# Optimization experiments

Hardware: AMD Instinct MI355X
Metric: run time of the kernel (lower is better)

## Reference

```python
import jax, jax.numpy as jnp
import numpy as np

B = 2048          # batch_size
D = 512           # embedding dim
TEMP = 0.1        # temperature
EPS = 1e-8        # torch CosineSimilarity eps


def _neg_idx(batch_size):
    n = 2 * batch_size
    mask = np.eye(n) + np.eye(n, n, k=-batch_size) + np.eye(n, n, k=batch_size)
    mask = (1 - mask).astype(bool)           # True at negatives
    # each row has exactly n-2 True entries -> fixed-shape gather indices
    return np.nonzero(mask)[1].reshape(n, n - 2)

_NEG_IDX = jnp.asarray(_neg_idx(B))           # [2B, 2B-2]
_ROWS = jnp.arange(2 * B)[:, None]            # [2B, 1]


def _cos_sim_matrix(r):
    # r: [2B, D] -> [2B, 2B] cosine similarity
    norm = jnp.maximum(jnp.linalg.norm(r, axis=-1, keepdims=True), EPS)
    rn = r / norm
    return rn @ rn.T


def _pos(sim):
    # diag(sim, +B) and diag(sim, -B), concatenated -> [2B, 1]
    l = jnp.diagonal(sim, offset=B)
    r = jnp.diagonal(sim, offset=-B)
    return jnp.concatenate([l, r])[:, None]


def _neg(sim):
    # masked gather of off-(diag,+B,-B) entries -> [2B, 2B-2]
    return sim[_ROWS, _NEG_IDX]


def _ce_sum_label0(logits):
    # CrossEntropyLoss(reduction='sum') with all labels == 0
    return -jnp.sum(jax.nn.log_softmax(logits, axis=-1)[:, 0])


def setup_inputs() -> dict:
    key = jax.random.key(0)
    k1, k2, k3, k4 = jax.random.split(key, 4)
    return {
        "z_ori": jax.random.normal(k1, (B, D), jnp.float32),
        "z_hard_pos": jax.random.normal(k2, (B, D), jnp.float32),
        "z_soft_pos": jax.random.normal(k3, (B, D), jnp.float32),
        "z_soft_neg": jax.random.normal(k4, (B, D), jnp.float32),
    }


def reference(z_ori, z_hard_pos, z_soft_pos, z_soft_neg):
    sim_ori_hp = _cos_sim_matrix(jnp.concatenate([z_ori, z_hard_pos], axis=0))
    sim_ori_sp = _cos_sim_matrix(jnp.concatenate([z_ori, z_soft_pos], axis=0))
    sim_ori_sn = _cos_sim_matrix(jnp.concatenate([z_ori, z_soft_neg], axis=0))
    sim_hp_sp = _cos_sim_matrix(jnp.concatenate([z_hard_pos, z_soft_pos], axis=0))
    sim_hp_sn = _cos_sim_matrix(jnp.concatenate([z_hard_pos, z_soft_neg], axis=0))
    sim_sp_sn = _cos_sim_matrix(jnp.concatenate([z_soft_pos, z_soft_neg], axis=0))

    pos_ori_sn = _pos(sim_ori_sn)
    pos_hp_sn = _pos(sim_hp_sn)
    pos_sp_sn = _pos(sim_sp_sn)

    pos_ori_hp = _pos(sim_ori_hp)
    neg_ori_hp = _neg(sim_ori_hp)
    pos_ori_sp = _pos(sim_ori_sp)
    neg_ori_sp = _neg(sim_ori_sp)
    pos_hp_sp = _pos(sim_hp_sp)
    neg_hp_sp = _neg(sim_hp_sp)

    logits_ori_hp = jnp.concatenate([pos_ori_hp, neg_ori_hp, pos_ori_sn], axis=1) / TEMP
    logits_ori_sp = jnp.concatenate([pos_ori_sp, neg_ori_sp, pos_ori_sn], axis=1) / TEMP
    logits_hp_sp = jnp.concatenate([pos_hp_sp, neg_hp_sp, pos_hp_sn, pos_sp_sn], axis=1) / TEMP

    denom = 2.0 * B
    return (
        _ce_sum_label0(logits_ori_hp) / denom,
        _ce_sum_label0(logits_ori_sp) / denom,
        _ce_sum_label0(logits_hp_sp) / denom,
    )
```

## Files before the change

### kernel.cpp

```cpp
#include <hip/hip_runtime.h>
#include <hip/hip_bf16.h>

#define Bn 2048
#define Dn 512

typedef float f32x4 __attribute__((ext_vector_type(4)));

typedef __attribute__((address_space(1))) const unsigned int gas_u32;
typedef __attribute__((address_space(3))) unsigned int las_u32;

__device__ __forceinline__ void gload16(const void* g, void* l) {
  __builtin_amdgcn_global_load_lds((gas_u32*)g, (las_u32*)l, 16, 0, 0);
}

__global__ __launch_bounds__(256) void normalize_kernel(
    const float* __restrict__ in0, const float* __restrict__ in1,
    const float* __restrict__ in2, const float* __restrict__ in3,
    unsigned char* __restrict__ nm8, float* __restrict__ rs, float* __restrict__ dd) {
  __shared__ float sv[4][Dn];
  __shared__ float red[4][6];
  int row = blockIdx.x;
  int wave = threadIdx.x >> 6, lane = threadIdx.x & 63;

  int g = blockIdx.x * 256 + threadIdx.x;
  if (g < 9 * Bn) rs[g] = 0.0f;

  const float* src =
      (wave == 0 ? in0 : wave == 1 ? in1 : wave == 2 ? in2 : in3) + (size_t)row * Dn;
  int k = lane * 8;
  float4 x0 = *(const float4*)(src + k);
  float4 x1 = *(const float4*)(src + k + 4);
  float v[8] = {x0.x, x0.y, x0.z, x0.w, x1.x, x1.y, x1.z, x1.w};
  float ss = 0.f;
#pragma unroll
  for (int e = 0; e < 8; e++) ss = fmaf(v[e], v[e], ss);
#pragma unroll
  for (int off = 1; off < 64; off <<= 1) ss += __shfl_xor(ss, off, 64);
  float scale = 1.0f / fmaxf(sqrtf(ss), 1e-8f);
  float nv[8];
#pragma unroll
  for (int e = 0; e < 8; e++) {
    nv[e] = v[e] * scale;
    sv[wave][k + e] = nv[e];
  }
  if (wave < 3) {
    unsigned int lo = __builtin_amdgcn_cvt_pk_fp8_f32(nv[0], nv[1], 0u, false);
    lo = __builtin_amdgcn_cvt_pk_fp8_f32(nv[2], nv[3], lo, true);
    unsigned int hi = __builtin_amdgcn_cvt_pk_fp8_f32(nv[4], nv[5], 0u, false);
    hi = __builtin_amdgcn_cvt_pk_fp8_f32(nv[6], nv[7], hi, true);
    uint2 pk; pk.x = lo; pk.y = hi;
    *(uint2*)(nm8 + ((size_t)wave * Bn + row) * Dn + k) = pk;
  }
  __syncthreads();

  int t = threadIdx.x;
  float o0 = sv[0][2 * t], o1 = sv[0][2 * t + 1];
  float h0 = sv[1][2 * t], h1 = sv[1][2 * t + 1];
  float p0 = sv[2][2 * t], p1 = sv[2][2 * t + 1];
  float n0 = sv[3][2 * t], n1 = sv[3][2 * t + 1];
  float s[6];
  s[0] = fmaf(o0, h0, o1 * h1);
  s[1] = fmaf(o0, p0, o1 * p1);
  s[2] = fmaf(h0, p0, h1 * p1);
  s[3] = fmaf(o0, n0, o1 * n1);
  s[4] = fmaf(h0, n0, h1 * n1);
  s[5] = fmaf(p0, n0, p1 * n1);
#pragma unroll
  for (int off = 1; off < 64; off <<= 1) {
#pragma unroll
    for (int j = 0; j < 6; j++) s[j] += __shfl_xor(s[j], off, 64);
  }
  if (lane == 0) {
#pragma unroll
    for (int j = 0; j < 6; j++) red[wave][j] = s[j];
  }
  __syncthreads();
  if (threadIdx.x < 6) {
    int j = threadIdx.x;
    dd[j * Bn + row] = red[0][j] + red[1][j] + red[2][j] + red[3][j];
  }
}

#define GBM 128
#define GBK 64
#define NKT 8
#define NBUF 3

__global__ __launch_bounds__(512, 6) void gemm_fp8_kernel(const unsigned char* __restrict__ nm8,
                                                          float* __restrict__ rs) {
  __shared__ unsigned char lds[NBUF * 16384];

  int id = ((int)blockIdx.x & 7) * 147 + ((int)blockIdx.x >> 3);
  int by = 0, rem = id, cnt = 48;
  while (rem >= cnt) { rem -= cnt; by++; cnt--; }
  int bx = by + rem;
  int u = by >> 4, v = bx >> 4;
  int rrow, rcol;
  if (u == v) { rrow = u; rcol = u; }
  else if (u == 0) { if (v == 1) { rrow = 3; rcol = 4; } else { rrow = 5; rcol = 6; } }
  else { rrow = 7; rcol = 8; }

  const unsigned char* gA = nm8 + ((size_t)u * Bn + (size_t)(by & 15) * GBM) * Dn;
  const unsigned char* gB = nm8 + ((size_t)v * Bn + (size_t)(bx & 15) * GBM) * Dn;

  int tid = threadIdx.x, lane = tid & 63, wave = tid >> 6;
  int wr = wave >> 2, wc = wave & 3;
  int c = lane & 15, rgrp = lane >> 4;
  int xc = ((c >> 1) & 3) << 1;

  int srow = tid >> 2;
  int sx = ((srow >> 1) & 3) << 1;
  int su = ((tid & 3) << 1) ^ sx;
  const unsigned char* sA = gA + (size_t)srow * Dn + su * 8;
  const unsigned char* sB = gB + (size_t)srow * Dn + su * 8;
  int woff = wave << 10;

  f32x4 acc[4][2] = {};

  gload16(sA, lds + woff);
  gload16(sB, lds + 8192 + woff);
  gload16(sA + GBK, lds + 16384 + woff);
  gload16(sB + GBK, lds + 16384 + 8192 + woff);
  asm volatile("s_waitcnt vmcnt(2)" ::: "memory");
  __builtin_amdgcn_s_barrier();
  asm volatile("" ::: "memory");

#pragma unroll
  for (int t = 0; t < NKT; ++t) {
    const int j = t % NBUF;
    const unsigned char* As = lds + j * 16384;
    const unsigned char* Bs = As + 8192;
    long long a[2][4], b[2][2];
#pragma unroll
    for (int ks = 0; ks < 2; ++ks) {
      int ub = (ks * 4 + rgrp) ^ xc;
#pragma unroll
      for (int mi = 0; mi < 4; ++mi)
        a[ks][mi] = *(const long long*)(As + (wr * 64 + mi * 16 + c) * 64 + ub * 8);
#pragma unroll
      for (int ni = 0; ni < 2; ++ni)
        b[ks][ni] = *(const long long*)(Bs + (wc * 32 + ni * 16 + c) * 64 + ub * 8);
    }
    if (t + 2 < NKT) {
      const int j2 = (t + 2) % NBUF;
      gload16(sA + (t + 2) * GBK, lds + j2 * 16384 + woff);
      gload16(sB + (t + 2) * GBK, lds + j2 * 16384 + 8192 + woff);
    }
    __builtin_amdgcn_s_setprio(1);
#pragma unroll
    for (int ks = 0; ks < 2; ++ks)
#pragma unroll
      for (int mi = 0; mi < 4; ++mi)
#pragma unroll
        for (int ni = 0; ni < 2; ++ni)
          acc[mi][ni] =
              __builtin_amdgcn_mfma_f32_16x16x32_fp8_fp8(a[ks][mi], b[ks][ni], acc[mi][ni], 0, 0, 0);
    __builtin_amdgcn_s_setprio(0);
    if (t + 2 < NKT) {
      asm volatile("s_waitcnt vmcnt(2)" ::: "memory");
    } else if (t == NKT - 2) {
      asm volatile("s_waitcnt vmcnt(0)" ::: "memory");
    }
    __builtin_amdgcn_s_barrier();
    asm volatile("" ::: "memory");
    __builtin_amdgcn_sched_barrier(0);
  }

  float* crow = (float*)lds;
  float* ccol = crow + GBM;
  __syncthreads();
  if (tid < 2 * GBM) ((float*)lds)[tid] = 0.0f;
  __syncthreads();

  bool skip_diag = (by == bx);
#pragma unroll
  for (int mi = 0; mi < 4; ++mi)
#pragma unroll
    for (int ni = 0; ni < 2; ++ni)
#pragma unroll
      for (int r = 0; r < 4; ++r) {
        int lrow = wr * 64 + mi * 16 + rgrp * 4 + r;
        int lcol = wc * 32 + ni * 16 + c;
        float e = __expf(10.0f * acc[mi][ni][r] - 10.0f);
        acc[mi][ni][r] = (skip_diag && lrow == lcol) ? 0.0f : e;
      }

#pragma unroll
  for (int mi = 0; mi < 4; ++mi)
#pragma unroll
    for (int r = 0; r < 4; ++r) {
      float val = acc[mi][0][r] + acc[mi][1][r];
      val += __shfl_xor(val, 1, 64);
      val += __shfl_xor(val, 2, 64);
      val += __shfl_xor(val, 4, 64);
      val += __shfl_xor(val, 8, 64);
      if (c == 0) atomicAdd(&crow[wr * 64 + mi * 16 + rgrp * 4 + r], val);
    }
#pragma unroll
  for (int ni = 0; ni < 2; ++ni) {
    float cv = 0.f;
#pragma unroll
    for (int mi = 0; mi < 4; ++mi)
#pragma unroll
      for (int r = 0; r < 4; ++r) cv += acc[mi][ni][r];
    cv += __shfl_xor(cv, 16, 64);
    cv += __shfl_xor(cv, 32, 64);
    if (lane < 16) atomicAdd(&ccol[wc * 32 + ni * 16 + c], cv);
  }
  __syncthreads();

  float* rs_row = rs + rrow * Bn + (by & 15) * GBM;
  if (tid < GBM) {
    atomicAdd(rs_row + tid, crow[tid]);
  } else if (tid < 2 * GBM && by != bx) {
    float* rs_col = rs + rcol * Bn + (bx & 15) * GBM;
    atomicAdd(rs_col + (tid - GBM), ccol[tid - GBM]);
  }
}

__global__ __launch_bounds__(1024) void final_kernel(const float* __restrict__ rs,
                                                     const float* __restrict__ dd,
                                                     float* __restrict__ out) {
  int tid = threadIdx.x;
  float l1 = 0.f, l2 = 0.f, l3 = 0.f;
  for (int i = tid; i < Bn; i += 1024) {
    float doh = dd[i], dop = dd[Bn + i], dhp = dd[2 * Bn + i];
    float ea = __expf(10.0f * dd[3 * Bn + i] - 10.0f);
    float eb = __expf(10.0f * dd[4 * Bn + i] - 10.0f);
    float ec = __expf(10.0f * dd[5 * Bn + i] - 10.0f);
    float r0 = rs[i], r1 = rs[Bn + i], r2 = rs[2 * Bn + i];
    float r3 = rs[3 * Bn + i], r4 = rs[4 * Bn + i], r5 = rs[5 * Bn + i];
    float r6 = rs[6 * Bn + i], r7 = rs[7 * Bn + i], r8 = rs[8 * Bn + i];
    l1 += 20.0f + logf(r0 + r3 + ea) + logf(r4 + r1 + ea) - 20.0f * doh;
    l2 += 20.0f + logf(r0 + r5 + ea) + logf(r6 + r2 + ea) - 20.0f * dop;
    l3 += 20.0f + logf(r1 + r7 + eb + ec) + logf(r8 + r2 + eb + ec) - 20.0f * dhp;
  }
  __shared__ float red[3][1024];
  red[0][tid] = l1; red[1][tid] = l2; red[2][tid] = l3;
  __syncthreads();
  for (int s = 512; s > 0; s >>= 1) {
    if (tid < s) {
      red[0][tid] += red[0][tid + s];
      red[1][tid] += red[1][tid + s];
      red[2][tid] += red[2][tid + s];
    }
    __syncthreads();
  }
  if (tid == 0) {
    out[0] = red[0][0] / 4096.0f;
    out[1] = red[1][0] / 4096.0f;
    out[2] = red[2][0] / 4096.0f;
  }
}

extern "C" void kernel_launch(void* const* d_in, const int* in_sizes, int n_in,
                              void* d_out, int out_size, void* d_ws, size_t ws_size,
                              hipStream_t stream) {
  const float* z0 = (const float*)d_in[0];
  const float* z1 = (const float*)d_in[1];
  const float* z2 = (const float*)d_in[2];
  const float* z3 = (const float*)d_in[3];
  float* out = (float*)d_out;

  unsigned char* nm8 = (unsigned char*)d_ws;
  float* rs = (float*)((char*)d_ws + (size_t)3 * Bn * Dn);
  float* dd = rs + 9 * Bn;

  hipLaunchKernelGGL(normalize_kernel, dim3(2048), dim3(256), 0, stream,
                     z0, z1, z2, z3, nm8, rs, dd);
  hipLaunchKernelGGL(gemm_fp8_kernel, dim3(1176), dim3(512), 0, stream, nm8, rs);
  hipLaunchKernelGGL(final_kernel, dim3(1), dim3(1024), 0, stream, rs, dd, out);
}
```

Before: 47.78 us.

## Enlarge FP8 GEMM tile to 256x256 with interleaved per-k-step MFMA scheduling

Doubles the GEMM block tile from 128x128 to 256x256, so each block holds an 8x4 accumulator grid per wave and loads four 16-byte chunks per stage. This cuts the grid from 1176 to 300 blocks and halves global/LDS traffic per output. The LDS fragment loads and MFMAs are now interleaved per k-substep, and blocks are remapped across XCDs. The cost is much higher register and LDS use (occupancy hint lowered to 2) and coarser load balance: 300 blocks on roughly 256 CUs leaves a partial second wave.

```diff
diff --git a/kernel.cpp b/kernel.cpp
--- a/kernel.cpp
+++ b/kernel.cpp
@@ -81,27 +81,30 @@
   }
 }
 
-#define GBM 128
+#define GBM 256
 #define GBK 64
 #define NKT 8
 #define NBUF 3
 
-__global__ __launch_bounds__(512, 6) void gemm_fp8_kernel(const unsigned char* __restrict__ nm8,
+__global__ __launch_bounds__(512, 2) void gemm_fp8_kernel(const unsigned char* __restrict__ nm8,
                                                           float* __restrict__ rs) {
-  __shared__ unsigned char lds[NBUF * 16384];
-
-  int id = ((int)blockIdx.x & 7) * 147 + ((int)blockIdx.x >> 3);
-  int by = 0, rem = id, cnt = 48;
+  __shared__ unsigned char lds[NBUF * 32768];
+
+  int orig = (int)blockIdx.x;
+  int xcd = orig & 7;
+  int id = (xcd < 4 ? xcd * 38 : 152 + (xcd - 4) * 37) + (orig >> 3);
+
+  int by = 0, rem = id, cnt = 24;
   while (rem >= cnt) { rem -= cnt; by++; cnt--; }
   int bx = by + rem;
-  int u = by >> 4, v = bx >> 4;
+  int u = by >> 3, v = bx >> 3;
   int rrow, rcol;
   if (u == v) { rrow = u; rcol = u; }
   else if (u == 0) { if (v == 1) { rrow = 3; rcol = 4; } else { rrow = 5; rcol = 6; } }
   else { rrow = 7; rcol = 8; }
 
-  const unsigned char* gA = nm8 + ((size_t)u * Bn + (size_t)(by & 15) * GBM) * Dn;
-  const unsigned char* gB = nm8 + ((size_t)v * Bn + (size_t)(bx & 15) * GBM) * Dn;
+  const unsigned char* gA = nm8 + ((size_t)u * Bn + (size_t)(by & 7) * GBM) * Dn;
+  const unsigned char* gB = nm8 + ((size_t)v * Bn + (size_t)(bx & 7) * GBM) * Dn;
 
   int tid = threadIdx.x, lane = tid & 63, wave = tid >> 6;
   int wr = wave >> 2, wc = wave & 3;
@@ -109,111 +112,113 @@
   int xc = ((c >> 1) & 3) << 1;
 
   int srow = tid >> 2;
-  int sx = ((srow >> 1) & 3) << 1;
-  int su = ((tid & 3) << 1) ^ sx;
-  const unsigned char* sA = gA + (size_t)srow * Dn + su * 8;
-  const unsigned char* sB = gB + (size_t)srow * Dn + su * 8;
-  int woff = wave << 10;
-
-  f32x4 acc[4][2] = {};
-
-  gload16(sA, lds + woff);
-  gload16(sB, lds + 8192 + woff);
-  gload16(sA + GBK, lds + 16384 + woff);
-  gload16(sB + GBK, lds + 16384 + 8192 + woff);
-  asm volatile("s_waitcnt vmcnt(2)" ::: "memory");
+  int suu = (tid & 3) ^ ((srow >> 1) & 3);
+  size_t aoff = (size_t)srow * Dn + suu * 16;
+  const unsigned char* sA = gA + aoff;
+  const unsigned char* sB = gB + aoff;
+  int dbase = wave << 10;
+
+#define STAGE(kt, j)                                                              \
+  {                                                                               \
+    unsigned char* d = lds + (j) * 32768;                                         \
+    gload16(sA + (kt) * GBK, d + dbase);                                          \
+    gload16(sA + (kt) * GBK + (size_t)128 * Dn, d + 8192 + dbase);                \
+    gload16(sB + (kt) * GBK, d + 16384 + dbase);                                  \
+    gload16(sB + (kt) * GBK + (size_t)128 * Dn, d + 16384 + 8192 + dbase);        \
+  }
+
+  f32x4 acc[8][4] = {};
+
+  STAGE(0, 0);
+  STAGE(1, 1);
+  asm volatile("s_waitcnt vmcnt(4)" ::: "memory");
   __builtin_amdgcn_s_barrier();
   asm volatile("" ::: "memory");
 
 #pragma unroll
   for (int t = 0; t < NKT; ++t) {
     const int j = t % NBUF;
-    const unsigned char* As = lds + j * 16384;
-    const unsigned char* Bs = As + 8192;
-    long long a[2][4], b[2][2];
+    const unsigned char* As = lds + j * 32768;
+    const unsigned char* Bs = As + 16384;
+    if (t + 2 < NKT) STAGE(t + 2, (t + 2) % NBUF);
 #pragma unroll
     for (int ks = 0; ks < 2; ++ks) {
-      int ub = (ks * 4 + rgrp) ^ xc;
-#pragma unroll
-      for (int mi = 0; mi < 4; ++mi)
-        a[ks][mi] = *(const long long*)(As + (wr * 64 + mi * 16 + c) * 64 + ub * 8);
-#pragma unroll
-      for (int ni = 0; ni < 2; ++ni)
-        b[ks][ni] = *(const long long*)(Bs + (wc * 32 + ni * 16 + c) * 64 + ub * 8);
+      int ub = ((ks * 4 + rgrp) ^ xc) << 3;
+      long long a[8], b[4];
+#pragma unroll
+      for (int mi = 0; mi < 8; ++mi)
+        a[mi] = *(const long long*)(As + (wr * 128 + mi * 16 + c) * 64 + ub);
+#pragma unroll
+      for (int ni = 0; ni < 4; ++ni)
+        b[ni] = *(const long long*)(Bs + (wc * 64 + ni * 16 + c) * 64 + ub);
+      __builtin_amdgcn_s_setprio(1);
+#pragma unroll
+      for (int mi = 0; mi < 8; ++mi)
+#pragma unroll
+        for (int ni = 0; ni < 4; ++ni)
+          acc[mi][ni] =
+              __builtin_amdgcn_mfma_f32_16x16x32_fp8_fp8(a[mi], b[ni], acc[mi][ni], 0, 0, 0);
+      __builtin_amdgcn_s_setprio(0);
     }
     if (t + 2 < NKT) {
-      const int j2 = (t + 2) % NBUF;
-      gload16(sA + (t + 2) * GBK, lds + j2 * 16384 + woff);
-      gload16(sB + (t + 2) * GBK, lds + j2 * 16384 + 8192 + woff);
-    }
-    __builtin_amdgcn_s_setprio(1);
-#pragma unroll
-    for (int ks = 0; ks < 2; ++ks)
-#pragma unroll
-      for (int mi = 0; mi < 4; ++mi)
-#pragma unroll
-        for (int ni = 0; ni < 2; ++ni)
-          acc[mi][ni] =
-              __builtin_amdgcn_mfma_f32_16x16x32_fp8_fp8(a[ks][mi], b[ks][ni], acc[mi][ni], 0, 0, 0);
-    __builtin_amdgcn_s_setprio(0);
-    if (t + 2 < NKT) {
-      asm volatile("s_waitcnt vmcnt(2)" ::: "memory");
-    } else if (t == NKT - 2) {
+      asm volatile("s_waitcnt vmcnt(4)" ::: "memory");
+    } else if (t + 1 < NKT) {
       asm volatile("s_waitcnt vmcnt(0)" ::: "memory");
     }
     __builtin_amdgcn_s_barrier();
     asm volatile("" ::: "memory");
     __builtin_amdgcn_sched_barrier(0);
   }
+#undef STAGE
 
   float* crow = (float*)lds;
   float* ccol = crow + GBM;
   __syncthreads();
-  if (tid < 2 * GBM) ((float*)lds)[tid] = 0.0f;
+  ((float*)lds)[tid] = 0.0f;
   __syncthreads();
 
   bool skip_diag = (by == bx);
 #pragma unroll
-  for (int mi = 0; mi < 4; ++mi)
-#pragma unroll
-    for (int ni = 0; ni < 2; ++ni)
+  for (int mi = 0; mi < 8; ++mi)
+#pragma unroll
+    for (int ni = 0; ni < 4; ++ni)
 #pragma unroll
       for (int r = 0; r < 4; ++r) {
-        int lrow = wr * 64 + mi * 16 + rgrp * 4 + r;
-        int lcol = wc * 32 + ni * 16 + c;
+        int lrow = wr * 128 + mi * 16 + rgrp * 4 + r;
+        int lcol = wc * 64 + ni * 16 + c;
         float e = __expf(10.0f * acc[mi][ni][r] - 10.0f);
         acc[mi][ni][r] = (skip_diag && lrow == lcol) ? 0.0f : e;
       }
 
 #pragma unroll
-  for (int mi = 0; mi < 4; ++mi)
+  for (int mi = 0; mi < 8; ++mi)
 #pragma unroll
     for (int r = 0; r < 4; ++r) {
-      float val = acc[mi][0][r] + acc[mi][1][r];
+      float val = acc[mi][0][r] + acc[mi][1][r] + acc[mi][2][r] + acc[mi][3][r];
       val += __shfl_xor(val, 1, 64);
       val += __shfl_xor(val, 2, 64);
       val += __shfl_xor(val, 4, 64);
       val += __shfl_xor(val, 8, 64);
-      if (c == 0) atomicAdd(&crow[wr * 64 + mi * 16 + rgrp * 4 + r], val);
-    }
-#pragma unroll
-  for (int ni = 0; ni < 2; ++ni) {
+      if (c == 0) atomicAdd(&crow[wr * 128 + mi * 16 + rgrp * 4 + r], val);
+    }
+#pragma unroll
+  for (int ni = 0; ni < 4; ++ni) {
     float cv = 0.f;
 #pragma unroll
-    for (int mi = 0; mi < 4; ++mi)
+    for (int mi = 0; mi < 8; ++mi)
 #pragma unroll
       for (int r = 0; r < 4; ++r) cv += acc[mi][ni][r];
     cv += __shfl_xor(cv, 16, 64);
     cv += __shfl_xor(cv, 32, 64);
-    if (lane < 16) atomicAdd(&ccol[wc * 32 + ni * 16 + c], cv);
-  }
-  __syncthreads();
-
-  float* rs_row = rs + rrow * Bn + (by & 15) * GBM;
+    if (lane < 16) atomicAdd(&ccol[wc * 64 + ni * 16 + c], cv);
+  }
+  __syncthreads();
+
+  float* rs_row = rs + rrow * Bn + (by & 7) * GBM;
   if (tid < GBM) {
     atomicAdd(rs_row + tid, crow[tid]);
-  } else if (tid < 2 * GBM && by != bx) {
-    float* rs_col = rs + rcol * Bn + (bx & 15) * GBM;
+  } else if (by != bx) {
+    float* rs_col = rs + rcol * Bn + (bx & 7) * GBM;
     atomicAdd(rs_col + (tid - GBM), ccol[tid - GBM]);
   }
 }
@@ -268,6 +273,6 @@
 
   hipLaunchKernelGGL(normalize_kernel, dim3(2048), dim3(256), 0, stream,
                      z0, z1, z2, z3, nm8, rs, dd);
-  hipLaunchKernelGGL(gemm_fp8_kernel, dim3(1176), dim3(512), 0, stream, nm8, rs);
+  hipLaunchKernelGGL(gemm_fp8_kernel, dim3(300), dim3(512), 0, stream, nm8, rs);
   hipLaunchKernelGGL(final_kernel, dim3(1), dim3(1024), 0, stream, rs, dd, out);
 }
```

Result: slower. 55.45 us (+16.0%).

## Permute fp8 layout for 16-byte LDS reads and deepen prefetch to four buffers

Applied to the files above, without the earlier changes.

The normalize kernel now writes fp8 rows in a permuted order within each 64-byte k-block, so each lane's two k-substeps sit next to each other. The GEMM can then fetch its A and B fragments with one 16-byte LDS read instead of two 8-byte reads, using a matching XOR swizzle. The pipeline grows from three to four LDS buffers with prefetch distance three, and the occupancy hint in launch_bounds is dropped. The goal is fewer LDS instructions and better hiding of global-to-LDS latency, at the cost of more LDS per block and possibly fewer resident blocks.

```diff
diff --git a/kernel.cpp b/kernel.cpp
--- a/kernel.cpp
+++ b/kernel.cpp
@@ -5,6 +5,7 @@
 #define Dn 512
 
 typedef float f32x4 __attribute__((ext_vector_type(4)));
+typedef long long ll2 __attribute__((ext_vector_type(2)));
 
 typedef __attribute__((address_space(1))) const unsigned int gas_u32;
 typedef __attribute__((address_space(3))) unsigned int las_u32;
@@ -22,8 +23,8 @@
   int row = blockIdx.x;
   int wave = threadIdx.x >> 6, lane = threadIdx.x & 63;
 
-  int g = blockIdx.x * 256 + threadIdx.x;
-  if (g < 9 * Bn) rs[g] = 0.0f;
+  int g0 = blockIdx.x * 256 + threadIdx.x;
+  if (g0 < 9 * Bn) rs[g0] = 0.0f;
 
   const float* src =
       (wave == 0 ? in0 : wave == 1 ? in1 : wave == 2 ? in2 : in3) + (size_t)row * Dn;
@@ -49,7 +50,9 @@
     unsigned int hi = __builtin_amdgcn_cvt_pk_fp8_f32(nv[4], nv[5], 0u, false);
     hi = __builtin_amdgcn_cvt_pk_fp8_f32(nv[6], nv[7], hi, true);
     uint2 pk; pk.x = lo; pk.y = hi;
-    *(uint2*)(nm8 + ((size_t)wave * Bn + row) * Dn + k) = pk;
+    int kb = lane >> 3, g = lane & 7;
+    int p = ((g & 3) << 1) | (g >> 2);
+    *(uint2*)(nm8 + ((size_t)wave * Bn + row) * Dn + kb * 64 + p * 8) = pk;
   }
   __syncthreads();
 
@@ -84,10 +87,10 @@
 #define GBM 128
 #define GBK 64
 #define NKT 8
-#define NBUF 3
-
-__global__ __launch_bounds__(512, 6) void gemm_fp8_kernel(const unsigned char* __restrict__ nm8,
-                                                          float* __restrict__ rs) {
+#define NBUF 4
+
+__global__ __launch_bounds__(512) void gemm_fp8_kernel(const unsigned char* __restrict__ nm8,
+                                                       float* __restrict__ rs) {
   __shared__ unsigned char lds[NBUF * 16384];
 
   int id = ((int)blockIdx.x & 7) * 147 + ((int)blockIdx.x >> 3);
@@ -106,46 +109,44 @@
   int tid = threadIdx.x, lane = tid & 63, wave = tid >> 6;
   int wr = wave >> 2, wc = wave & 3;
   int c = lane & 15, rgrp = lane >> 4;
-  int xc = ((c >> 1) & 3) << 1;
+  int ru = ((rgrp ^ ((c >> 1) & 3)) << 4);
 
   int srow = tid >> 2;
-  int sx = ((srow >> 1) & 3) << 1;
-  int su = ((tid & 3) << 1) ^ sx;
-  const unsigned char* sA = gA + (size_t)srow * Dn + su * 8;
-  const unsigned char* sB = gB + (size_t)srow * Dn + su * 8;
-  int woff = wave << 10;
+  int suu = (tid & 3) ^ ((srow >> 1) & 3);
+  size_t aoff = (size_t)srow * Dn + suu * 16;
+  const unsigned char* sA = gA + aoff;
+  const unsigned char* sB = gB + aoff;
+  int dbase = wave << 10;
+
+#define STAGE(kt, j)                                         \
+  {                                                          \
+    unsigned char* d = lds + (j) * 16384;                    \
+    gload16(sA + (kt) * GBK, d + dbase);                     \
+    gload16(sB + (kt) * GBK, d + 8192 + dbase);              \
+  }
 
   f32x4 acc[4][2] = {};
 
-  gload16(sA, lds + woff);
-  gload16(sB, lds + 8192 + woff);
-  gload16(sA + GBK, lds + 16384 + woff);
-  gload16(sB + GBK, lds + 16384 + 8192 + woff);
-  asm volatile("s_waitcnt vmcnt(2)" ::: "memory");
+  STAGE(0, 0);
+  STAGE(1, 1);
+  STAGE(2, 2);
+  asm volatile("s_waitcnt vmcnt(4)" ::: "memory");
   __builtin_amdgcn_s_barrier();
   asm volatile("" ::: "memory");
 
 #pragma unroll
   for (int t = 0; t < NKT; ++t) {
-    const int j = t % NBUF;
-    const unsigned char* As = lds + j * 16384;
+    const unsigned char* As = lds + (t & 3) * 16384;
     const unsigned char* Bs = As + 8192;
-    long long a[2][4], b[2][2];
-#pragma unroll
-    for (int ks = 0; ks < 2; ++ks) {
-      int ub = (ks * 4 + rgrp) ^ xc;
-#pragma unroll
-      for (int mi = 0; mi < 4; ++mi)
-        a[ks][mi] = *(const long long*)(As + (wr * 64 + mi * 16 + c) * 64 + ub * 8);
-#pragma unroll
-      for (int ni = 0; ni < 2; ++ni)
-        b[ks][ni] = *(const long long*)(Bs + (wc * 32 + ni * 16 + c) * 64 + ub * 8);
-    }
-    if (t + 2 < NKT) {
-      const int j2 = (t + 2) % NBUF;
-      gload16(sA + (t + 2) * GBK, lds + j2 * 16384 + woff);
-      gload16(sB + (t + 2) * GBK, lds + j2 * 16384 + 8192 + woff);
-    }
+    if (t + 3 < NKT) STAGE(t + 3, (t + 3) & 3);
+    ll2 a[4];
+    ll2 b[2];
+#pragma unroll
+    for (int mi = 0; mi < 4; ++mi)
+      a[mi] = *(const ll2*)(As + (wr * 64 + mi * 16 + c) * 64 + ru);
+#pragma unroll
+    for (int ni = 0; ni < 2; ++ni)
+      b[ni] = *(const ll2*)(Bs + (wc * 32 + ni * 16 + c) * 64 + ru);
     __builtin_amdgcn_s_setprio(1);
 #pragma unroll
     for (int ks = 0; ks < 2; ++ks)
@@ -154,17 +155,20 @@
 #pragma unroll
         for (int ni = 0; ni < 2; ++ni)
           acc[mi][ni] =
-              __builtin_amdgcn_mfma_f32_16x16x32_fp8_fp8(a[ks][mi], b[ks][ni], acc[mi][ni], 0, 0, 0);
+              __builtin_amdgcn_mfma_f32_16x16x32_fp8_fp8(a[mi][ks], b[ni][ks], acc[mi][ni], 0, 0, 0);
     __builtin_amdgcn_s_setprio(0);
-    if (t + 2 < NKT) {
+    if (t + 3 < NKT) {
+      asm volatile("s_waitcnt vmcnt(4)" ::: "memory");
+    } else if (t + 2 < NKT) {
       asm volatile("s_waitcnt vmcnt(2)" ::: "memory");
-    } else if (t == NKT - 2) {
+    } else if (t + 1 < NKT) {
       asm volatile("s_waitcnt vmcnt(0)" ::: "memory");
     }
     __builtin_amdgcn_s_barrier();
     asm volatile("" ::: "memory");
     __builtin_amdgcn_sched_barrier(0);
   }
+#undef STAGE
 
   float* crow = (float*)lds;
   float* ccol = crow + GBM;
```

New measurement: 44.83 us. 1.07x faster.
